# Kernel tuning notes

Measured on AMD Instinct MI355X. Metric: run time of the kernel, lower is better.

## Reference

```python
import jax, jax.numpy as jnp
import numpy as np

H_MAX = 0.05
TIME_LEN = 5  # t = linspace(0, 1, 5); uniform segments of length 0.25
N_STEPS = int(np.ceil(0.25 / H_MAX))  # Euler steps per segment = 5 (matches torch ode_solve)


def setup_inputs() -> dict:
    key = jax.random.key(0)
    k1, k2, k3, k4, k5 = jax.random.split(key, 5)
    bs, d, hidden = 1024, 1024, 2048
    z0 = jax.random.normal(k1, (bs, d), dtype=jnp.float32)
    t = jnp.linspace(0.0, 1.0, TIME_LEN).astype(jnp.float32)
    # MLP ODEF params: f(z, t) = tanh([z, t] @ W1 + b1) @ W2 + b2
    s1 = 1.0 / np.sqrt(d + 1)
    s2 = 1.0 / np.sqrt(hidden)
    W1 = jax.random.uniform(k2, (d + 1, hidden), jnp.float32, -s1, s1)
    b1 = jax.random.uniform(k3, (hidden,), jnp.float32, -s1, s1)
    W2 = jax.random.uniform(k4, (hidden, d), jnp.float32, -s2, s2)
    b2 = jax.random.uniform(k5, (d,), jnp.float32, -s2, s2)
    return {"z0": z0, "t": t, "W1": W1, "b1": b1, "W2": W2, "b2": b2}


def _f(z, t_scalar, W1, b1, W2, b2):
    # z: [bs, d]; t_scalar broadcast as an extra input feature
    bs = z.shape[0]
    zt = jnp.concatenate([z, jnp.full((bs, 1), t_scalar, dtype=z.dtype)], axis=1)
    h = jnp.tanh(zt @ W1 + b1)
    return h @ W2 + b2


def _ode_solve(z0, t0, t1, W1, b1, W2, b2):
    # Euler: z <- z + h * f(z, t), N_STEPS fixed steps (h_max = 0.05)
    h = (t1 - t0) / N_STEPS

    def step(carry, _):
        z, t = carry
        z = z + h * _f(z, t, W1, b1, W2, b2)
        return (z, t + h), None

    (z, _), _ = jax.lax.scan(step, (z0, t0), None, length=N_STEPS)
    return z


def reference(z0, t, W1, b1, W2, b2):
    # NeuralODE.forward with return_whole_sequence=False: returns z at final time point.
    z = z0
    for i in range(TIME_LEN - 1):  # small fixed loop over time checkpoints
        z = _ode_solve(z, t[i], t[i + 1], W1, b1, W2, b2)
    return z
```

## Files before the change

### kernel.cpp

```cpp
#include <hip/hip_runtime.h>
#include <cstdint>
#include <cstddef>


typedef __bf16 bf16x8 __attribute__((ext_vector_type(8)));
typedef float f32x4 __attribute__((ext_vector_type(4)));

#define WAITV(N) asm volatile("s_waitcnt vmcnt(" #N ") lgkmcnt(0)" ::: "memory")
#define BARRIER() asm volatile("s_barrier" ::: "memory")
#define SEP() asm volatile("" ::: "memory")

__device__ __forceinline__ unsigned short f2bf(float f) {
  union { float f; unsigned u; } v; v.f = f;
  unsigned r = v.u + 0x7fffu + ((v.u >> 16) & 1u);
  return (unsigned short)(r >> 16);
}

__device__ __forceinline__ float fast_tanh(float x) {
  float e = __builtin_amdgcn_exp2f(x * 2.8853900817779268f);
  return 1.0f - 2.0f * __builtin_amdgcn_rcpf(1.0f + e);
}

__global__ void transpose_to_bf16(const float* __restrict__ in,
                                  unsigned short* __restrict__ out,
                                  int rows, int cols) {
  __shared__ float tile[32][33];
  int c0 = blockIdx.x * 32, r0 = blockIdx.y * 32;
  int tx = threadIdx.x, ty = threadIdx.y;
#pragma unroll
  for (int j = 0; j < 32; j += 8)
    tile[ty + j][tx] = in[(size_t)(r0 + ty + j) * cols + (c0 + tx)];
  __syncthreads();
#pragma unroll
  for (int j = 0; j < 32; j += 8)
    out[(size_t)(c0 + ty + j) * rows + (r0 + tx)] = f2bf(tile[tx][ty + j]);
}

__global__ void prep_misc(const float* __restrict__ z0,
                          float* __restrict__ zf,
                          unsigned short* __restrict__ zbf,
                          const float* __restrict__ W1,
                          float* __restrict__ w1l, int n, int nl) {
  int i = blockIdx.x * blockDim.x + threadIdx.x;
  if (i < n) { float v = z0[i]; zf[i] = v; zbf[i] = f2bf(v); }
  if (i < nl) { w1l[i] = W1[(size_t)1024 * 2048 + i]; }
}

__device__ __forceinline__ void stage64(const unsigned short* __restrict__ g,
                                        size_t ld, int row0, int k0,
                                        unsigned short* lp, int tid) {
  int r = tid >> 3;
  int c = (tid & 7) ^ (r & 7);
  __builtin_amdgcn_global_load_lds(
      (const __attribute__((address_space(1))) void*)(
          g + (size_t)(row0 + r) * ld + k0 + c * 8),
      (__attribute__((address_space(3))) void*)(lp + tid * 8), 16, 0, 0);
}

__device__ __forceinline__ bf16x8 frag_ld(const unsigned short* lp, int row,
                                          int chunk_logical, int x) {
  return *(const bf16x8*)(lp + row * 64 + ((chunk_logical ^ x) << 3));
}

__global__ __launch_bounds__(512, 1) void gemm1_kernel(
    const unsigned short* __restrict__ Zb,
    const unsigned short* __restrict__ W1T,
    unsigned short* __restrict__ H,
    const float* __restrict__ b1, const float* __restrict__ w1l, float tval) {
  __shared__ __align__(16) unsigned short lds[36864];
  const int tid = threadIdx.x;
  const int lane = tid & 63, wid = tid >> 6;
  const int l15 = lane & 15, q = lane >> 4, x = l15 & 7;
  const int bid = blockIdx.x;
  const int xcd = bid & 7, loc = bid >> 3;
  const int mt = (loc & 3) | ((xcd & 3) << 2);
  const int nt = (loc >> 2) | ((xcd >> 2) << 3);
  const int m0 = mt * 64, n0 = nt * 128;

  unsigned short* const buf0 = lds;
  unsigned short* const buf1 = lds + 12288;
  unsigned short* const buf2 = lds + 24576;

  f32x4 acc[2][2] = {};

  auto stage_tile = [&](int t, unsigned short* p) {
    int k = t * 64;
    stage64(Zb, 1024, m0, k, p, tid);
    stage64(W1T, 1024, n0, k, p + 4096, tid);
    stage64(W1T, 1024, n0 + 64, k, p + 8192, tid);
  };
  auto compute = [&](const unsigned short* p) {
    const unsigned short* A = p + (wid & 1) * 2048;
    const unsigned short* B = p + 4096 + (wid >> 1) * 2048;
#pragma unroll
    for (int kk = 0; kk < 2; ++kk) {
      bf16x8 a[2], bb[2];
#pragma unroll
      for (int im = 0; im < 2; ++im)
        a[im] = frag_ld(A, im * 16 + l15, (kk << 2) + q, x);
#pragma unroll
      for (int jn = 0; jn < 2; ++jn)
        bb[jn] = frag_ld(B, jn * 16 + l15, (kk << 2) + q, x);
#pragma unroll
      for (int im = 0; im < 2; ++im)
#pragma unroll
        for (int jn = 0; jn < 2; ++jn)
          acc[im][jn] = __builtin_amdgcn_mfma_f32_16x16x32_bf16(
              a[im], bb[jn], acc[im][jn], 0, 0, 0);
    }
  };

#define STEP(t, pc, pn) \
  WAITV(3);             \
  BARRIER();            \
  stage_tile((t) + 2, pn); \
  compute(pc)

  stage_tile(0, buf0);
  SEP();
  stage_tile(1, buf1);

  STEP(0, buf0, buf2);
  STEP(1, buf1, buf0);
  STEP(2, buf2, buf1);
  STEP(3, buf0, buf2);
  STEP(4, buf1, buf0);
  STEP(5, buf2, buf1);
  STEP(6, buf0, buf2);
  STEP(7, buf1, buf0);
  STEP(8, buf2, buf1);
  STEP(9, buf0, buf2);
  STEP(10, buf1, buf0);
  STEP(11, buf2, buf1);
  STEP(12, buf0, buf2);
  STEP(13, buf1, buf0);
  WAITV(3);
  BARRIER();
  compute(buf2);
  WAITV(0);
  BARRIER();
  compute(buf0);
#undef STEP

#pragma unroll
  for (int jn = 0; jn < 2; ++jn) {
    int col = n0 + (wid >> 1) * 32 + jn * 16 + l15;
    float bb = b1[col] + tval * w1l[col];
#pragma unroll
    for (int im = 0; im < 2; ++im) {
      int rowb = m0 + (wid & 1) * 32 + im * 16 + q * 4;
#pragma unroll
      for (int r = 0; r < 4; ++r)
        H[(size_t)(rowb + r) * 2048 + col] =
            f2bf(fast_tanh(acc[im][jn][r] + bb));
    }
  }
}

__global__ __launch_bounds__(512, 1) void gemm2_kernel(
    const unsigned short* __restrict__ Hb,
    const unsigned short* __restrict__ W2T,
    const float* __restrict__ b2,
    const float* __restrict__ zf,
    float* __restrict__ outf,
    unsigned short* __restrict__ zbf,
    float h) {
  __shared__ __align__(16) unsigned short lds[49152];
  const int tid = threadIdx.x;
  const int lane = tid & 63, wid = tid >> 6;
  const int l15 = lane & 15, q = lane >> 4, x = l15 & 7;
  const int kh = wid >> 2, mh = (wid >> 1) & 1, nh = wid & 1;
  const int bid = blockIdx.x;
  const int xcd = bid & 7, loc = bid >> 3;
  const int mt = (loc & 3) | ((xcd & 3) << 2);
  const int nt = (loc >> 2) | ((xcd >> 2) << 3);
  const int m0 = mt * 64, n0 = nt * 64;

  unsigned short* const buf0 = lds;
  unsigned short* const buf1 = lds + 16384;
  unsigned short* const buf2 = lds + 32768;

  f32x4 acc[2][2] = {};

  auto stage_tile = [&](int t, unsigned short* p) {
    int k = t * 64;
    stage64(Hb, 2048, m0, k, p, tid);
    stage64(Hb, 2048, m0, k + 1024, p + 4096, tid);
    stage64(W2T, 2048, n0, k, p + 8192, tid);
    stage64(W2T, 2048, n0, k + 1024, p + 12288, tid);
  };
  auto compute = [&](const unsigned short* p) {
    const unsigned short* A = p + kh * 4096 + mh * 2048;
    const unsigned short* B = p + 8192 + kh * 4096 + nh * 2048;
#pragma unroll
    for (int kk = 0; kk < 2; ++kk) {
      bf16x8 a[2], bb[2];
#pragma unroll
      for (int im = 0; im < 2; ++im)
        a[im] = frag_ld(A, im * 16 + l15, (kk << 2) + q, x);
#pragma unroll
      for (int jn = 0; jn < 2; ++jn)
        bb[jn] = frag_ld(B, jn * 16 + l15, (kk << 2) + q, x);
#pragma unroll
      for (int im = 0; im < 2; ++im)
#pragma unroll
        for (int jn = 0; jn < 2; ++jn)
          acc[im][jn] = __builtin_amdgcn_mfma_f32_16x16x32_bf16(
              a[im], bb[jn], acc[im][jn], 0, 0, 0);
    }
  };

#define STEP(t, pc, pn) \
  WAITV(4);             \
  BARRIER();            \
  stage_tile((t) + 2, pn); \
  compute(pc)

  stage_tile(0, buf0);
  SEP();
  stage_tile(1, buf1);

  STEP(0, buf0, buf2);
  STEP(1, buf1, buf0);
  STEP(2, buf2, buf1);
  STEP(3, buf0, buf2);
  STEP(4, buf1, buf0);
  STEP(5, buf2, buf1);
  STEP(6, buf0, buf2);
  STEP(7, buf1, buf0);
  STEP(8, buf2, buf1);
  STEP(9, buf0, buf2);
  STEP(10, buf1, buf0);
  STEP(11, buf2, buf1);
  STEP(12, buf0, buf2);
  STEP(13, buf1, buf0);
  WAITV(4);
  BARRIER();
  compute(buf2);
  WAITV(0);
  BARRIER();
  compute(buf0);
#undef STEP

  __syncthreads();
  float* red = (float*)lds;
  const int region = (mh * 2 + nh) * 1056;
  if (kh == 1) {
#pragma unroll
    for (int im = 0; im < 2; ++im)
#pragma unroll
      for (int jn = 0; jn < 2; ++jn) {
        int c = jn * 16 + l15;
#pragma unroll
        for (int r = 0; r < 4; ++r)
          red[region + (im * 16 + q * 4 + r) * 33 + c] = acc[im][jn][r];
      }
  }
  __syncthreads();
  if (kh == 0) {
#pragma unroll
    for (int jn = 0; jn < 2; ++jn) {
      int coll = nh * 32 + jn * 16 + l15;
      int col = n0 + coll;
      float bb = b2[col];
#pragma unroll
      for (int im = 0; im < 2; ++im) {
        int rowl = im * 16 + q * 4;
#pragma unroll
        for (int r = 0; r < 4; ++r) {
          float s = acc[im][jn][r] +
                    red[region + (rowl + r) * 33 + jn * 16 + l15];
          size_t gidx = (size_t)(m0 + mh * 32 + rowl + r) * 1024 + col;
          float zv = zf[gidx] + h * (s + bb);
          outf[gidx] = zv;
          zbf[gidx] = f2bf(zv);
        }
      }
    }
  }
}

extern "C" void kernel_launch(void* const* d_in, const int* in_sizes, int n_in,
                              void* d_out, int out_size, void* d_ws,
                              size_t ws_size, hipStream_t stream) {
  const float* z0 = (const float*)d_in[0];
  const float* W1 = (const float*)d_in[2];
  const float* b1 = (const float*)d_in[3];
  const float* W2 = (const float*)d_in[4];
  const float* b2 = (const float*)d_in[5];
  float* out = (float*)d_out;

  char* ws = (char*)d_ws;
  unsigned short* W1T = (unsigned short*)(ws + 0);
  unsigned short* W2T = (unsigned short*)(ws + (4u << 20));
  unsigned short* zbf = (unsigned short*)(ws + (8u << 20));
  unsigned short* Hbf = (unsigned short*)(ws + (10u << 20));
  float* zf = (float*)(ws + (14u << 20));
  float* w1l = (float*)(ws + (18u << 20));

  transpose_to_bf16<<<dim3(64, 32), dim3(32, 8), 0, stream>>>(W1, W1T, 1024, 2048);
  transpose_to_bf16<<<dim3(32, 64), dim3(32, 8), 0, stream>>>(W2, W2T, 2048, 1024);
  prep_misc<<<4096, 256, 0, stream>>>(z0, zf, zbf, W1, w1l, 1024 * 1024, 2048);

  const float h = 0.05f;
  for (int seg = 0; seg < 4; ++seg) {
    float tcur = 0.25f * (float)seg;
    for (int j = 0; j < 5; ++j) {
      gemm1_kernel<<<256, 512, 0, stream>>>(zbf, W1T, Hbf, b1, w1l, tcur);
      bool last = (seg == 3 && j == 4);
      float* outf = last ? out : zf;
      gemm2_kernel<<<256, 512, 0, stream>>>(Hbf, W2T, b2, zf, outf, zbf, h);
      tcur += h;
    }
  }
}
```

Baseline: 432.3 us.

## Split K across warps in both GEMMs with LDS reduction of partial sums

Both GEMM kernels now give each warp a 32x64 output sub-tile and divide the K dimension of every staged tile between warp groups: two-way in gemm1, four-way in gemm2. Partial accumulators are summed through padded LDS buffers before the epilogue. The aim is more MFMAs per fragment load, since each B fragment is reused across more MFMAs and LDS read traffic per MFMA drops. The cost is an extra LDS reduction with two barriers, and only a subset of warps run the epilogue.

```diff
diff --git a/kernel.cpp b/kernel.cpp
--- a/kernel.cpp
+++ b/kernel.cpp
@@ -71,6 +71,7 @@
   const int tid = threadIdx.x;
   const int lane = tid & 63, wid = tid >> 6;
   const int l15 = lane & 15, q = lane >> 4, x = l15 & 7;
+  const int kh = wid >> 2, mh = (wid >> 1) & 1, nh2 = wid & 1;
   const int bid = blockIdx.x;
   const int xcd = bid & 7, loc = bid >> 3;
   const int mt = (loc & 3) | ((xcd & 3) << 2);
@@ -81,7 +82,7 @@
   unsigned short* const buf1 = lds + 12288;
   unsigned short* const buf2 = lds + 24576;
 
-  f32x4 acc[2][2] = {};
+  f32x4 acc[2][4] = {};
 
   auto stage_tile = [&](int t, unsigned short* p) {
     int k = t * 64;
@@ -90,24 +91,22 @@
     stage64(W1T, 1024, n0 + 64, k, p + 8192, tid);
   };
   auto compute = [&](const unsigned short* p) {
-    const unsigned short* A = p + (wid & 1) * 2048;
-    const unsigned short* B = p + 4096 + (wid >> 1) * 2048;
-#pragma unroll
-    for (int kk = 0; kk < 2; ++kk) {
-      bf16x8 a[2], bb[2];
-#pragma unroll
-      for (int im = 0; im < 2; ++im)
-        a[im] = frag_ld(A, im * 16 + l15, (kk << 2) + q, x);
-#pragma unroll
-      for (int jn = 0; jn < 2; ++jn)
-        bb[jn] = frag_ld(B, jn * 16 + l15, (kk << 2) + q, x);
-#pragma unroll
-      for (int im = 0; im < 2; ++im)
-#pragma unroll
-        for (int jn = 0; jn < 2; ++jn)
-          acc[im][jn] = __builtin_amdgcn_mfma_f32_16x16x32_bf16(
-              a[im], bb[jn], acc[im][jn], 0, 0, 0);
-    }
+    const unsigned short* A = p + mh * 2048;
+    const unsigned short* B = p + 4096 + nh2 * 4096;
+    const int cb = (kh << 2) + q;
+    bf16x8 a[2], bb[4];
+#pragma unroll
+    for (int im = 0; im < 2; ++im)
+      a[im] = frag_ld(A, im * 16 + l15, cb, x);
+#pragma unroll
+    for (int jn = 0; jn < 4; ++jn)
+      bb[jn] = frag_ld(B, jn * 16 + l15, cb, x);
+#pragma unroll
+    for (int im = 0; im < 2; ++im)
+#pragma unroll
+      for (int jn = 0; jn < 4; ++jn)
+        acc[im][jn] = __builtin_amdgcn_mfma_f32_16x16x32_bf16(
+            a[im], bb[jn], acc[im][jn], 0, 0, 0);
   };
 
 #define STEP(t, pc, pn) \
@@ -142,17 +141,35 @@
   compute(buf0);
 #undef STEP
 
-#pragma unroll
-  for (int jn = 0; jn < 2; ++jn) {
-    int col = n0 + (wid >> 1) * 32 + jn * 16 + l15;
-    float bb = b1[col] + tval * w1l[col];
-#pragma unroll
-    for (int im = 0; im < 2; ++im) {
-      int rowb = m0 + (wid & 1) * 32 + im * 16 + q * 4;
-#pragma unroll
-      for (int r = 0; r < 4; ++r)
-        H[(size_t)(rowb + r) * 2048 + col] =
-            f2bf(fast_tanh(acc[im][jn][r] + bb));
+  __syncthreads();
+  float* red = (float*)lds;
+  const int region = (mh * 2 + nh2) * 2080;
+  if (kh == 1) {
+#pragma unroll
+    for (int im = 0; im < 2; ++im)
+#pragma unroll
+      for (int jn = 0; jn < 4; ++jn)
+#pragma unroll
+        for (int r = 0; r < 4; ++r)
+          red[region + (im * 16 + q * 4 + r) * 65 + jn * 16 + l15] =
+              acc[im][jn][r];
+  }
+  __syncthreads();
+  if (kh == 0) {
+#pragma unroll
+    for (int jn = 0; jn < 4; ++jn) {
+      int col = n0 + nh2 * 64 + jn * 16 + l15;
+      float bb = b1[col] + tval * w1l[col];
+#pragma unroll
+      for (int im = 0; im < 2; ++im) {
+        int rowb = m0 + mh * 32 + im * 16 + q * 4;
+#pragma unroll
+        for (int r = 0; r < 4; ++r) {
+          float s = acc[im][jn][r] +
+                    red[region + (im * 16 + q * 4 + r) * 65 + jn * 16 + l15];
+          H[(size_t)(rowb + r) * 2048 + col] = f2bf(fast_tanh(s + bb));
+        }
+      }
     }
   }
 }
@@ -169,7 +186,7 @@
   const int tid = threadIdx.x;
   const int lane = tid & 63, wid = tid >> 6;
   const int l15 = lane & 15, q = lane >> 4, x = l15 & 7;
-  const int kh = wid >> 2, mh = (wid >> 1) & 1, nh = wid & 1;
+  const int kh = wid >> 1, mh = wid & 1;
   const int bid = blockIdx.x;
   const int xcd = bid & 7, loc = bid >> 3;
   const int mt = (loc & 3) | ((xcd & 3) << 2);
@@ -180,7 +197,7 @@
   unsigned short* const buf1 = lds + 16384;
   unsigned short* const buf2 = lds + 32768;
 
-  f32x4 acc[2][2] = {};
+  f32x4 acc[2][4] = {};
 
   auto stage_tile = [&](int t, unsigned short* p) {
     int k = t * 64;
@@ -190,24 +207,22 @@
     stage64(W2T, 2048, n0, k + 1024, p + 12288, tid);
   };
   auto compute = [&](const unsigned short* p) {
-    const unsigned short* A = p + kh * 4096 + mh * 2048;
-    const unsigned short* B = p + 8192 + kh * 4096 + nh * 2048;
-#pragma unroll
-    for (int kk = 0; kk < 2; ++kk) {
-      bf16x8 a[2], bb[2];
-#pragma unroll
-      for (int im = 0; im < 2; ++im)
-        a[im] = frag_ld(A, im * 16 + l15, (kk << 2) + q, x);
-#pragma unroll
-      for (int jn = 0; jn < 2; ++jn)
-        bb[jn] = frag_ld(B, jn * 16 + l15, (kk << 2) + q, x);
-#pragma unroll
-      for (int im = 0; im < 2; ++im)
-#pragma unroll
-        for (int jn = 0; jn < 2; ++jn)
-          acc[im][jn] = __builtin_amdgcn_mfma_f32_16x16x32_bf16(
-              a[im], bb[jn], acc[im][jn], 0, 0, 0);
-    }
+    const unsigned short* A = p + (kh >> 1) * 4096 + mh * 2048;
+    const unsigned short* B = p + 8192 + (kh >> 1) * 4096;
+    const int cb = ((kh & 1) << 2) + q;
+    bf16x8 a[2], bb[4];
+#pragma unroll
+    for (int im = 0; im < 2; ++im)
+      a[im] = frag_ld(A, im * 16 + l15, cb, x);
+#pragma unroll
+    for (int jn = 0; jn < 4; ++jn)
+      bb[jn] = frag_ld(B, jn * 16 + l15, cb, x);
+#pragma unroll
+    for (int im = 0; im < 2; ++im)
+#pragma unroll
+      for (int jn = 0; jn < 4; ++jn)
+        acc[im][jn] = __builtin_amdgcn_mfma_f32_16x16x32_bf16(
+            a[im], bb[jn], acc[im][jn], 0, 0, 0);
   };
 
 #define STEP(t, pc, pn) \
@@ -244,32 +259,34 @@
 
   __syncthreads();
   float* red = (float*)lds;
-  const int region = (mh * 2 + nh) * 1056;
-  if (kh == 1) {
-#pragma unroll
-    for (int im = 0; im < 2; ++im)
-#pragma unroll
-      for (int jn = 0; jn < 2; ++jn) {
-        int c = jn * 16 + l15;
+  if (kh != 0) {
+    const int region = ((kh - 1) * 2 + mh) * 2080;
+#pragma unroll
+    for (int im = 0; im < 2; ++im)
+#pragma unroll
+      for (int jn = 0; jn < 4; ++jn)
 #pragma unroll
         for (int r = 0; r < 4; ++r)
-          red[region + (im * 16 + q * 4 + r) * 33 + c] = acc[im][jn][r];
-      }
+          red[region + (im * 16 + q * 4 + r) * 65 + jn * 16 + l15] =
+              acc[im][jn][r];
   }
   __syncthreads();
   if (kh == 0) {
-#pragma unroll
-    for (int jn = 0; jn < 2; ++jn) {
-      int coll = nh * 32 + jn * 16 + l15;
-      int col = n0 + coll;
+    const int r0g = (0 * 2 + mh) * 2080;
+    const int r1g = (1 * 2 + mh) * 2080;
+    const int r2g = (2 * 2 + mh) * 2080;
+#pragma unroll
+    for (int jn = 0; jn < 4; ++jn) {
+      int col = n0 + jn * 16 + l15;
       float bb = b2[col];
 #pragma unroll
       for (int im = 0; im < 2; ++im) {
         int rowl = im * 16 + q * 4;
 #pragma unroll
         for (int r = 0; r < 4; ++r) {
-          float s = acc[im][jn][r] +
-                    red[region + (rowl + r) * 33 + jn * 16 + l15];
+          int off = (rowl + r) * 65 + jn * 16 + l15;
+          float s = acc[im][jn][r] + red[r0g + off] + red[r1g + off] +
+                    red[r2g + off];
           size_t gidx = (size_t)(m0 + mh * 32 + rowl + r) * 1024 + col;
           float zv = zf[gidx] + h * (s + bb);
           outf[gidx] = zv;
```

After: 474.7 us. 1.1x slower.

## Double gemm1 K-tile to 128 and fuse prep kernels into one launch

Applied to the files above, without the earlier changes.

The gemm1 kernel now stages K=128 per pipeline stage instead of 64, doubling LDS use to 144KB across three buffers. This halves the number of barrier/wait iterations, and the vmcnt wait is raised to match the six loads in flight. The two transpose kernels and the misc prep kernel are merged into a single launch to cut launch overhead. The larger LDS footprint and longer stages may change latency hiding and occupancy.

```diff
diff --git a/kernel.cpp b/kernel.cpp
--- a/kernel.cpp
+++ b/kernel.cpp
@@ -21,29 +21,41 @@
   return 1.0f - 2.0f * __builtin_amdgcn_rcpf(1.0f + e);
 }
 
-__global__ void transpose_to_bf16(const float* __restrict__ in,
-                                  unsigned short* __restrict__ out,
-                                  int rows, int cols) {
+__global__ void prep_all(const float* __restrict__ W1,
+                         const float* __restrict__ W2,
+                         unsigned short* __restrict__ W1T,
+                         unsigned short* __restrict__ W2T,
+                         const float* __restrict__ z0,
+                         float* __restrict__ zf,
+                         unsigned short* __restrict__ zbf,
+                         float* __restrict__ w1l) {
   __shared__ float tile[32][33];
-  int c0 = blockIdx.x * 32, r0 = blockIdx.y * 32;
-  int tx = threadIdx.x, ty = threadIdx.y;
-#pragma unroll
-  for (int j = 0; j < 32; j += 8)
-    tile[ty + j][tx] = in[(size_t)(r0 + ty + j) * cols + (c0 + tx)];
-  __syncthreads();
-#pragma unroll
-  for (int j = 0; j < 32; j += 8)
-    out[(size_t)(c0 + ty + j) * rows + (r0 + tx)] = f2bf(tile[tx][ty + j]);
-}
-
-__global__ void prep_misc(const float* __restrict__ z0,
-                          float* __restrict__ zf,
-                          unsigned short* __restrict__ zbf,
-                          const float* __restrict__ W1,
-                          float* __restrict__ w1l, int n, int nl) {
-  int i = blockIdx.x * blockDim.x + threadIdx.x;
-  if (i < n) { float v = z0[i]; zf[i] = v; zbf[i] = f2bf(v); }
-  if (i < nl) { w1l[i] = W1[(size_t)1024 * 2048 + i]; }
+  const int b = blockIdx.x;
+  const int tid = threadIdx.x;
+  const int tx = tid & 31, ty = tid >> 5;
+  if (b < 4096) {
+    const bool w1 = (b < 2048);
+    const float* in = w1 ? W1 : W2;
+    unsigned short* out = w1 ? W1T : W2T;
+    const int rows = w1 ? 1024 : 2048;
+    const int cols = w1 ? 2048 : 1024;
+    const int bb = w1 ? b : b - 2048;
+    const int c0 = w1 ? (bb & 63) * 32 : (bb & 31) * 32;
+    const int r0 = w1 ? (bb >> 6) * 32 : (bb >> 5) * 32;
+#pragma unroll
+    for (int j = 0; j < 32; j += 8)
+      tile[ty + j][tx] = in[(size_t)(r0 + ty + j) * cols + (c0 + tx)];
+    __syncthreads();
+#pragma unroll
+    for (int j = 0; j < 32; j += 8)
+      out[(size_t)(c0 + ty + j) * rows + (r0 + tx)] = f2bf(tile[tx][ty + j]);
+  } else {
+    const int i = (b - 4096) * 256 + tid;
+    float v = z0[i];
+    zf[i] = v;
+    zbf[i] = f2bf(v);
+    if (i < 2048) w1l[i] = W1[(size_t)1024 * 2048 + i];
+  }
 }
 
 __device__ __forceinline__ void stage64(const unsigned short* __restrict__ g,
@@ -67,7 +79,7 @@
     const unsigned short* __restrict__ W1T,
     unsigned short* __restrict__ H,
     const float* __restrict__ b1, const float* __restrict__ w1l, float tval) {
-  __shared__ __align__(16) unsigned short lds[36864];
+  __shared__ __align__(16) unsigned short lds[73728];
   const int tid = threadIdx.x;
   const int lane = tid & 63, wid = tid >> 6;
   const int l15 = lane & 15, q = lane >> 4, x = l15 & 7;
@@ -78,29 +90,35 @@
   const int m0 = mt * 64, n0 = nt * 128;
 
   unsigned short* const buf0 = lds;
-  unsigned short* const buf1 = lds + 12288;
-  unsigned short* const buf2 = lds + 24576;
+  unsigned short* const buf1 = lds + 24576;
+  unsigned short* const buf2 = lds + 49152;
 
   f32x4 acc[2][2] = {};
 
   auto stage_tile = [&](int t, unsigned short* p) {
-    int k = t * 64;
+    int k = t * 128;
     stage64(Zb, 1024, m0, k, p, tid);
-    stage64(W1T, 1024, n0, k, p + 4096, tid);
-    stage64(W1T, 1024, n0 + 64, k, p + 8192, tid);
+    stage64(Zb, 1024, m0, k + 64, p + 4096, tid);
+    stage64(W1T, 1024, n0, k, p + 8192, tid);
+    stage64(W1T, 1024, n0 + 64, k, p + 12288, tid);
+    stage64(W1T, 1024, n0, k + 64, p + 16384, tid);
+    stage64(W1T, 1024, n0 + 64, k + 64, p + 20480, tid);
   };
   auto compute = [&](const unsigned short* p) {
-    const unsigned short* A = p + (wid & 1) * 2048;
-    const unsigned short* B = p + 4096 + (wid >> 1) * 2048;
-#pragma unroll
-    for (int kk = 0; kk < 2; ++kk) {
+    const unsigned short* A0 = p + (wid & 1) * 2048;
+    const unsigned short* B0 = p + 8192 + (wid >> 1) * 2048;
+#pragma unroll
+    for (int kk = 0; kk < 4; ++kk) {
+      const unsigned short* A = A0 + (kk >> 1) * 4096;
+      const unsigned short* B = B0 + (kk >> 1) * 8192;
+      const int cb = ((kk & 1) << 2) + q;
       bf16x8 a[2], bb[2];
 #pragma unroll
       for (int im = 0; im < 2; ++im)
-        a[im] = frag_ld(A, im * 16 + l15, (kk << 2) + q, x);
+        a[im] = frag_ld(A, im * 16 + l15, cb, x);
 #pragma unroll
       for (int jn = 0; jn < 2; ++jn)
-        bb[jn] = frag_ld(B, jn * 16 + l15, (kk << 2) + q, x);
+        bb[jn] = frag_ld(B, jn * 16 + l15, cb, x);
 #pragma unroll
       for (int im = 0; im < 2; ++im)
 #pragma unroll
@@ -111,7 +129,7 @@
   };
 
 #define STEP(t, pc, pn) \
-  WAITV(3);             \
+  WAITV(6);             \
   BARRIER();            \
   stage_tile((t) + 2, pn); \
   compute(pc)
@@ -126,20 +144,12 @@
   STEP(3, buf0, buf2);
   STEP(4, buf1, buf0);
   STEP(5, buf2, buf1);
-  STEP(6, buf0, buf2);
-  STEP(7, buf1, buf0);
-  STEP(8, buf2, buf1);
-  STEP(9, buf0, buf2);
-  STEP(10, buf1, buf0);
-  STEP(11, buf2, buf1);
-  STEP(12, buf0, buf2);
-  STEP(13, buf1, buf0);
-  WAITV(3);
+  WAITV(6);
   BARRIER();
-  compute(buf2);
+  compute(buf0);
   WAITV(0);
   BARRIER();
-  compute(buf0);
+  compute(buf1);
 #undef STEP
 
 #pragma unroll
@@ -298,9 +308,7 @@
   float* zf = (float*)(ws + (14u << 20));
   float* w1l = (float*)(ws + (18u << 20));
 
-  transpose_to_bf16<<<dim3(64, 32), dim3(32, 8), 0, stream>>>(W1, W1T, 1024, 2048);
-  transpose_to_bf16<<<dim3(32, 64), dim3(32, 8), 0, stream>>>(W2, W2T, 2048, 1024);
-  prep_misc<<<4096, 256, 0, stream>>>(z0, zf, zbf, W1, w1l, 1024 * 1024, 2048);
+  prep_all<<<8192, 256, 0, stream>>>(W1, W2, W1T, W2T, z0, zf, zbf, w1l);
 
   const float h = 0.05f;
   for (int seg = 0; seg < 4; ++seg) {
```

Result: no change. 436.9 us (+1.1%).
